# Performance work log

Hardware: AMD Instinct MI355X
Metric: run time of the kernel (lower is better)

The kernel has to match this reference:

```python
import jax, jax.numpy as jnp
import numpy as np

IN_CH = 256
HID = 32
OUT_CH = 32
EPS = 1e-5


def setup_inputs() -> dict:
    key = jax.random.key(0)
    ks = jax.random.split(key, 7)
    B, L = 1, 256
    x = jax.random.normal(ks[0], (B, L, IN_CH), dtype=jnp.float32)
    # nn.Linear(in_channels, hidden_dim)
    W1 = jax.random.normal(ks[1], (IN_CH, HID), dtype=jnp.float32) / np.sqrt(IN_CH)
    b1 = jnp.zeros((HID,), dtype=jnp.float32)
    # nn.LayerNorm(hidden_dim * hidden_dim)
    gamma = jnp.ones((HID * HID,), dtype=jnp.float32)
    beta = jnp.zeros((HID * HID,), dtype=jnp.float32)
    # nn.Linear(hidden_dim * hidden_dim, out_channels)
    W2 = jax.random.normal(ks[2], (HID * HID, OUT_CH), dtype=jnp.float32) / np.sqrt(HID * HID)
    b2 = jnp.zeros((OUT_CH,), dtype=jnp.float32)
    return {"x": x, "W1": W1, "b1": b1, "gamma": gamma, "beta": beta, "W2": W2, "b2": b2}


def reference(x, W1, b1, gamma, beta, W2, b2):
    # a: [B, L, HID]
    a = jnp.einsum('bic,ch->bih', x, W1) + b1
    # outer product: [B, I, J, D, E] -> flatten to [B, I, J, D*E]
    outer = jnp.einsum('bid,bje->bijde', a, a)
    B, I, J, D, E = outer.shape
    outer = outer.reshape(B, I, J, D * E)
    # LayerNorm over last dim
    mu = jnp.mean(outer, axis=-1, keepdims=True)
    var = jnp.mean(jnp.square(outer - mu), axis=-1, keepdims=True)
    normed = (outer - mu) * jax.lax.rsqrt(var + EPS) * gamma + beta
    # final projection: [B, I, J, OUT_CH]
    return jnp.einsum('bijk,ko->bijo', normed, W2) + b2
```

## Files before the change

kernel.cpp:

```cpp
#include <hip/hip_runtime.h>

#define LSEQ 256
#define INC  256
#define HID  32
#define OUTC 32
#define DE   1024
#define EPSV 1e-5f

__global__ __launch_bounds__(256) void k1_a_stats(
    const float* __restrict__ x, const float* __restrict__ W1, const float* __restrict__ b1,
    const float* __restrict__ gamma, const float* __restrict__ beta,
    const float* __restrict__ W2, const float* __restrict__ b2,
    float* __restrict__ a, float* __restrict__ S, float* __restrict__ Q,
    float* __restrict__ GW, float* __restrict__ C)
{
    __shared__ float sh0[256];
    __shared__ float sh1[256];
    const int t = threadIdx.x;
    const int b = blockIdx.x;
    if (b < 32) {
        const int i = b * 8 + (t >> 5);
        const int d = t & 31;
        const float* xr = x + i * INC;
        float acc = b1[d];
        #pragma unroll 8
        for (int c = 0; c < INC; ++c)
            acc = fmaf(xr[c], W1[c * HID + d], acc);
        a[i * HID + d] = acc;
        sh0[t] = acc;
        sh1[t] = acc * acc;
        __syncthreads();
        if (t < 8) {
            float s = 0.f, q = 0.f;
            #pragma unroll
            for (int d2 = 0; d2 < 32; ++d2) { s += sh0[t * 32 + d2]; q += sh1[t * 32 + d2]; }
            S[b * 8 + t] = s;
            Q[b * 8 + t] = q;
        }
    } else {
        const int o = t & 31, chunk = t >> 5;
        float gw = 0.f, bw = 0.f;
        for (int k = 0; k < 128; ++k) {
            const int de = chunk * 128 + k;
            const float w = W2[de * OUTC + o];
            gw = fmaf(gamma[de], w, gw);
            bw = fmaf(beta[de],  w, bw);
        }
        sh0[t] = gw; sh1[t] = bw;
        __syncthreads();
        if (t < 32) {
            float g = 0.f, bb = 0.f;
            #pragma unroll
            for (int c2 = 0; c2 < 8; ++c2) { g += sh0[c2 * 32 + t]; bb += sh1[c2 * 32 + t]; }
            GW[t] = g;
            C[t]  = bb + b2[t];
        }
    }
}

__global__ __launch_bounds__(1024) void k2_T(
    const float* __restrict__ a, const float* __restrict__ gamma,
    const float* __restrict__ W2, float* __restrict__ T)
{
    const int j = blockIdx.x, t = threadIdx.x;
    __shared__ float aj[HID];
    if (t < HID) aj[t] = a[j * HID + t];
    __syncthreads();
    const int d = t >> 5, o = t & 31;
    float acc = 0.f;
    #pragma unroll
    for (int e = 0; e < 32; ++e) {
        const int de = d * 32 + e;
        acc = fmaf(aj[e] * gamma[de], W2[de * OUTC + o], acc);
    }
    T[j * DE + t] = acc;
}

__global__ __launch_bounds__(256) void k3_out(
    const float* __restrict__ a, const float* __restrict__ S, const float* __restrict__ Q,
    const float* __restrict__ GW, const float* __restrict__ C,
    const float* __restrict__ T, float* __restrict__ out)
{
    const int j = blockIdx.x, t = threadIdx.x;
    __shared__ float aL[LSEQ * HID];
    __shared__ float tL[DE];
    __shared__ float sL[LSEQ];
    __shared__ float qL[LSEQ];
    __shared__ float gwL[OUTC], cL[OUTC];

    for (int k = t; k < LSEQ * HID; k += 256) aL[k] = a[k];
    for (int k = t; k < DE; k += 256)         tL[k] = T[j * DE + k];
    sL[t] = S[t];
    qL[t] = Q[t];
    if (t < OUTC) { gwL[t] = GW[t]; cL[t] = C[t]; }
    __syncthreads();

    const int o  = t & 31;
    const int i0 = t >> 5;
    const float Sj = sL[j], Qj = qL[j];
    const float gw = gwL[o], cc = cL[o];

    for (int rep = 0; rep < 32; ++rep) {
        const int i = rep * 8 + i0;
        float acc = 0.f;
        #pragma unroll
        for (int d = 0; d < 32; ++d)
            acc = fmaf(aL[i * HID + d], tL[d * 32 + o], acc);
        const float Si = sL[i], Qi = qL[i];
        const float mu  = Si * Sj * (1.0f / 1024.0f);
        const float ex2 = Qi * Qj * (1.0f / 1024.0f);
        const float var = ex2 - mu * mu;
        const float r   = rsqrtf(var + EPSV);
        out[(i * LSEQ + j) * OUTC + o] = r * (acc - mu * gw) + cc;
    }
}

extern "C" void kernel_launch(void* const* d_in, const int* in_sizes, int n_in,
                              void* d_out, int out_size, void* d_ws, size_t ws_size,
                              hipStream_t stream)
{
    const float* x     = (const float*)d_in[0];
    const float* W1    = (const float*)d_in[1];
    const float* b1    = (const float*)d_in[2];
    const float* gamma = (const float*)d_in[3];
    const float* beta  = (const float*)d_in[4];
    const float* W2    = (const float*)d_in[5];
    const float* b2    = (const float*)d_in[6];
    float* out = (float*)d_out;

    float* ws = (float*)d_ws;
    float* a  = ws;
    float* S  = ws + 8192;
    float* Q  = ws + 8448;
    float* GW = ws + 8704;
    float* C  = ws + 8736;
    float* T  = ws + 8768;

    k1_a_stats<<<33, 256, 0, stream>>>(x, W1, b1, gamma, beta, W2, b2, a, S, Q, GW, C);
    k2_T<<<LSEQ, 1024, 0, stream>>>(a, gamma, W2, T);
    k3_out<<<LSEQ, 256, 0, stream>>>(a, S, Q, GW, C, T, out);
}
```

Measured before the change: 88.43 us.

## Fuse T computation into output kernel with register-tiled padded-LDS matmul

Merges the T-building kernel into the output kernel, so T lives in shared memory instead of a global round trip, and removes one launch. The output loop now gives each thread an 8x4 register tile read from a padded, transposed copy of a in LDS, with float4 stores. The first kernel splits the W1 reduction over two half-rows using 65 blocks to spread that work wider. The trade is more LDS and registers per block, which could lower occupancy.

New measurement: 80.65 us. 8.8% less time.

```diff
diff --git a/kernel.cpp b/kernel.cpp
--- a/kernel.cpp
+++ b/kernel.cpp
@@ -6,6 +6,9 @@
 #define OUTC 32
 #define DE   1024
 #define EPSV 1e-5f
+
+#define ASTR 260
+#define TSTR 36
 
 __global__ __launch_bounds__(256) void k1_a_stats(
     const float* __restrict__ x, const float* __restrict__ W1, const float* __restrict__ b1,
@@ -16,26 +19,38 @@
 {
     __shared__ float sh0[256];
     __shared__ float sh1[256];
+    __shared__ float shA[128];
+    __shared__ float shB[128];
     const int t = threadIdx.x;
     const int b = blockIdx.x;
-    if (b < 32) {
-        const int i = b * 8 + (t >> 5);
+    if (b < 64) {
+        const int r = t >> 6;
+        const int h = (t >> 5) & 1;
         const int d = t & 31;
-        const float* xr = x + i * INC;
-        float acc = b1[d];
+        const int i = b * 4 + r;
+        const float* xr = x + i * INC + h * 128;
+        const float* w  = W1 + (h * 128) * HID + d;
+        float p0 = 0.f, p1 = 0.f;
         #pragma unroll 8
-        for (int c = 0; c < INC; ++c)
-            acc = fmaf(xr[c], W1[c * HID + d], acc);
-        a[i * HID + d] = acc;
-        sh0[t] = acc;
-        sh1[t] = acc * acc;
+        for (int k = 0; k < 64; ++k) {
+            p0 = fmaf(xr[2 * k],     w[(2 * k) * HID],     p0);
+            p1 = fmaf(xr[2 * k + 1], w[(2 * k + 1) * HID], p1);
+        }
+        sh0[t] = p0 + p1;
         __syncthreads();
-        if (t < 8) {
+        if (h == 0) {
+            const float tot = sh0[t] + sh0[t + 32] + b1[d];
+            a[i * HID + d] = tot;
+            shA[r * 32 + d] = tot;
+            shB[r * 32 + d] = tot * tot;
+        }
+        __syncthreads();
+        if (t < 4) {
             float s = 0.f, q = 0.f;
             #pragma unroll
-            for (int d2 = 0; d2 < 32; ++d2) { s += sh0[t * 32 + d2]; q += sh1[t * 32 + d2]; }
-            S[b * 8 + t] = s;
-            Q[b * 8 + t] = q;
+            for (int d2 = 0; d2 < 32; ++d2) { s += shA[t * 32 + d2]; q += shB[t * 32 + d2]; }
+            S[b * 4 + t] = s;
+            Q[b * 4 + t] = q;
         }
     } else {
         const int o = t & 31, chunk = t >> 5;
@@ -58,60 +73,99 @@
     }
 }
 
-__global__ __launch_bounds__(1024) void k2_T(
-    const float* __restrict__ a, const float* __restrict__ gamma,
-    const float* __restrict__ W2, float* __restrict__ T)
+__global__ __launch_bounds__(256) void k2_fused(
+    const float* __restrict__ a, const float* __restrict__ S, const float* __restrict__ Q,
+    const float* __restrict__ GW, const float* __restrict__ C,
+    const float* __restrict__ gamma, const float* __restrict__ W2,
+    float* __restrict__ out)
 {
     const int j = blockIdx.x, t = threadIdx.x;
-    __shared__ float aj[HID];
-    if (t < HID) aj[t] = a[j * HID + t];
-    __syncthreads();
-    const int d = t >> 5, o = t & 31;
-    float acc = 0.f;
-    #pragma unroll
-    for (int e = 0; e < 32; ++e) {
-        const int de = d * 32 + e;
-        acc = fmaf(aj[e] * gamma[de], W2[de * OUTC + o], acc);
-    }
-    T[j * DE + t] = acc;
-}
-
-__global__ __launch_bounds__(256) void k3_out(
-    const float* __restrict__ a, const float* __restrict__ S, const float* __restrict__ Q,
-    const float* __restrict__ GW, const float* __restrict__ C,
-    const float* __restrict__ T, float* __restrict__ out)
-{
-    const int j = blockIdx.x, t = threadIdx.x;
-    __shared__ float aL[LSEQ * HID];
-    __shared__ float tL[DE];
+    __shared__ float aPad[32 * ASTR];
+    __shared__ float tPad[32 * TSTR];
+    __shared__ float gL[DE];
     __shared__ float sL[LSEQ];
     __shared__ float qL[LSEQ];
     __shared__ float gwL[OUTC], cL[OUTC];
 
-    for (int k = t; k < LSEQ * HID; k += 256) aL[k] = a[k];
-    for (int k = t; k < DE; k += 256)         tL[k] = T[j * DE + k];
+    {
+        const float4* ar4 = (const float4*)(a + t * HID);
+        const int base = (t >> 3) * ASTR + (t & 7);
+        #pragma unroll
+        for (int c = 0; c < 8; ++c) {
+            const float4 v = ar4[c];
+            const int d = c * 4;
+            aPad[base + (d + 0) * 8] = v.x;
+            aPad[base + (d + 1) * 8] = v.y;
+            aPad[base + (d + 2) * 8] = v.z;
+            aPad[base + (d + 3) * 8] = v.w;
+        }
+    }
+    #pragma unroll
+    for (int k = t; k < DE; k += 256) gL[k] = gamma[k];
     sL[t] = S[t];
     qL[t] = Q[t];
     if (t < OUTC) { gwL[t] = GW[t]; cL[t] = C[t]; }
     __syncthreads();
 
-    const int o  = t & 31;
-    const int i0 = t >> 5;
+    {
+        const int d = t >> 3, o0 = (t & 7) * 4;
+        const int jb = (j >> 3) * ASTR + (j & 7);
+        float4 acc = {0.f, 0.f, 0.f, 0.f};
+        #pragma unroll
+        for (int e = 0; e < 32; ++e) {
+            const float g = gL[d * 32 + e] * aPad[jb + e * 8];
+            const float4 w = *(const float4*)(W2 + (d * 32 + e) * OUTC + o0);
+            acc.x = fmaf(g, w.x, acc.x);
+            acc.y = fmaf(g, w.y, acc.y);
+            acc.z = fmaf(g, w.z, acc.z);
+            acc.w = fmaf(g, w.w, acc.w);
+        }
+        *(float4*)(tPad + d * TSTR + o0) = acc;
+    }
+    __syncthreads();
+
+    const int iT = t >> 3, oT = t & 7;
+    const int abase = iT * ASTR;
+    float acc[8][4];
+    #pragma unroll
+    for (int m = 0; m < 8; ++m)
+        #pragma unroll
+        for (int k = 0; k < 4; ++k) acc[m][k] = 0.f;
+
+    #pragma unroll
+    for (int d = 0; d < 32; ++d) {
+        const float4 a0 = *(const float4*)(aPad + abase + d * 8);
+        const float4 a1 = *(const float4*)(aPad + abase + d * 8 + 4);
+        const float4 tf = *(const float4*)(tPad + d * TSTR + oT * 4);
+        const float am[8] = {a0.x, a0.y, a0.z, a0.w, a1.x, a1.y, a1.z, a1.w};
+        const float tk[4] = {tf.x, tf.y, tf.z, tf.w};
+        #pragma unroll
+        for (int m = 0; m < 8; ++m)
+            #pragma unroll
+            for (int k = 0; k < 4; ++k)
+                acc[m][k] = fmaf(am[m], tk[k], acc[m][k]);
+    }
+
     const float Sj = sL[j], Qj = qL[j];
-    const float gw = gwL[o], cc = cL[o];
+    const float gw0 = gwL[oT * 4 + 0], gw1 = gwL[oT * 4 + 1];
+    const float gw2 = gwL[oT * 4 + 2], gw3 = gwL[oT * 4 + 3];
+    const float c0 = cL[oT * 4 + 0], c1 = cL[oT * 4 + 1];
+    const float c2 = cL[oT * 4 + 2], c3 = cL[oT * 4 + 3];
 
-    for (int rep = 0; rep < 32; ++rep) {
-        const int i = rep * 8 + i0;
-        float acc = 0.f;
-        #pragma unroll
-        for (int d = 0; d < 32; ++d)
-            acc = fmaf(aL[i * HID + d], tL[d * 32 + o], acc);
+    #pragma unroll
+    for (int m = 0; m < 8; ++m) {
+        const int i = iT * 8 + m;
         const float Si = sL[i], Qi = qL[i];
         const float mu  = Si * Sj * (1.0f / 1024.0f);
         const float ex2 = Qi * Qj * (1.0f / 1024.0f);
         const float var = ex2 - mu * mu;
         const float r   = rsqrtf(var + EPSV);
-        out[(i * LSEQ + j) * OUTC + o] = r * (acc - mu * gw) + cc;
+        float4 o4;
+        o4.x = fmaf(r, acc[m][0] - mu * gw0, c0);
+        o4.y = fmaf(r, acc[m][1] - mu * gw1, c1);
+        o4.z = fmaf(r, acc[m][2] - mu * gw2, c2);
+        o4.w = fmaf(r, acc[m][3] - mu * gw3, c3);
+        *(float4*)(out + (i * LSEQ + j) * OUTC + oT * 4) = o4;
     }
 }
 
@@ -134,9 +188,7 @@
     float* Q  = ws + 8448;
     float* GW = ws + 8704;
     float* C  = ws + 8736;
-    float* T  = ws + 8768;
 
-    k1_a_stats<<<33, 256, 0, stream>>>(x, W1, b1, gamma, beta, W2, b2, a, S, Q, GW, C);
-    k2_T<<<LSEQ, 1024, 0, stream>>>(a, gamma, W2, T);
-    k3_out<<<LSEQ, 256, 0, stream>>>(a, S, Q, GW, C, T, out);
+    k1_a_stats<<<65, 256, 0, stream>>>(x, W1, b1, gamma, beta, W2, b2, a, S, Q, GW, C);
+    k2_fused<<<LSEQ, 256, 0, stream>>>(a, S, Q, GW, C, gamma, W2, out);
 }
```
